# Kernel optimization log

Measured on AMD Instinct MI355X. Metric: run time of the kernel, lower is better.

## Reference

```python
import jax, jax.numpy as jnp
import numpy as np

NUM_GROUPS = 4   # temporal frames == deformable groups
K = 3            # deformable / fusion kernel size
PAD = 1
MAX_DISP = 7
STRIDE2 = 2


def _conv2d(x, w):
    # 3x3, stride 1, pad 1, no bias, NCHW/OIHW
    return jax.lax.conv_general_dilated(
        x, w, window_strides=(1, 1), padding=((PAD, PAD), (PAD, PAD)),
        dimension_numbers=("NCHW", "OIHW", "NCHW"))


def _correlation(x1, x2):
    """FlowNet/PWC correlation: kernel_size=1, max_displacement=7, stride1=1, stride2=2.
    Output: [B, 49, H, W], mean over channels of shifted dot products."""
    B, C, H, W = x1.shape
    r = MAX_DISP // STRIDE2          # 3 -> 7x7 displacement grid
    m = r * STRIDE2                  # 6 = max shift magnitude
    x2p = jnp.pad(x2, ((0, 0), (0, 0), (m, m), (m, m)))
    outs = []
    for di in range(-r, r + 1):
        for dj in range(-r, r + 1):
            dy, dx = di * STRIDE2, dj * STRIDE2
            sh = x2p[:, :, m + dy:m + dy + H, m + dx:m + dx + W]
            outs.append(jnp.mean(x1 * sh, axis=1))
    return jnp.stack(outs, axis=1)   # [B, 49, H, W]


def _deform_conv(x, offset, weight):
    """Deformable conv v1 (ConvOffset2d): 3x3, stride 1, pad 1, NUM_GROUPS deformable groups.
    offset: [B, G*2*K*K, H, W] laid out as (g, k, {dy,dx})."""
    B, C, H, W = x.shape
    G, K2 = NUM_GROUPS, K * K
    Cg = C // G
    off = offset.reshape(B, G, K2, 2, H, W)
    rel = (jnp.arange(K) - PAD).astype(x.dtype)
    rel_y = jnp.repeat(rel, K).reshape(1, 1, K2, 1, 1)   # kh-major, matches weight flatten
    rel_x = jnp.tile(rel, K).reshape(1, 1, K2, 1, 1)
    iy = jnp.arange(H, dtype=x.dtype).reshape(1, 1, 1, H, 1)
    ix = jnp.arange(W, dtype=x.dtype).reshape(1, 1, 1, 1, W)
    py = iy + rel_y + off[:, :, :, 0]   # [B,G,K2,H,W] sample rows
    px = ix + rel_x + off[:, :, :, 1]   # sample cols
    xg = x.reshape(B, G, Cg, H, W).transpose(0, 1, 3, 4, 2)  # [B,G,H,W,Cg]
    y0 = jnp.floor(py); x0 = jnp.floor(px)
    fy = py - y0; fx = px - x0
    y0 = y0.astype(jnp.int32); x0 = x0.astype(jnp.int32)
    bi = jnp.arange(B).reshape(B, 1, 1, 1, 1)
    gi = jnp.arange(G).reshape(1, G, 1, 1, 1)
    acc = jnp.zeros((B, G, K2, H, W, Cg), x.dtype)
    for dy in (0, 1):
        for dx in (0, 1):
            yy = y0 + dy; xx = x0 + dx
            wgt = (fy if dy else 1.0 - fy) * (fx if dx else 1.0 - fx)
            valid = ((yy >= 0) & (yy < H) & (xx >= 0) & (xx < W)).astype(x.dtype)
            v = xg[bi, gi, jnp.clip(yy, 0, H - 1), jnp.clip(xx, 0, W - 1)]
            acc = acc + v * (wgt * valid)[..., None]
    wr = weight.reshape(weight.shape[0], G, Cg, K2)  # [O,G,Cg,K2]
    return jnp.einsum('bgkhwc,ogck->bohw', acc, wr)


def setup_inputs() -> dict:
    key = jax.random.key(0)
    k0, k1, k2, k3 = jax.random.split(key, 4)
    B, C, H, W = 4, 256, 64, 64
    G = NUM_GROUPS
    inputs = jax.random.normal(k0, (B * G, C, H, W), jnp.float32)
    w_offset = jax.random.normal(k1, (G * 2 * K * K, C + MAX_DISP ** 2, K, K), jnp.float32) * 0.02
    w_def = jax.random.normal(k2, (C, C, K, K), jnp.float32) * 0.02
    w_fusion = jax.random.normal(k3, (C, C * G, K, K), jnp.float32) * 0.02
    return {"inputs": inputs, "w_offset": w_offset, "w_def": w_def,
            "w_fusion": w_fusion, "d1": 0, "d2": 0}


def reference(inputs, w_offset, w_def, w_fusion, d1, d2):
    # d1, d2 are unused by the original forward.
    G = NUM_GROUPS
    y = inputs[G - 1::G]
    _y = jax.lax.stop_gradient(y)
    feats = []
    for ii in range(G - 1):           # n_iter = 1
        x = inputs[ii::G]
        _x = jax.lax.stop_gradient(x)
        corr = _correlation(_x, _y)                       # [B,49,H,W]
        off = _conv2d(jnp.concatenate([x, corr], axis=1), w_offset)
        x = _deform_conv(x, off, w_def)
        feats.append(x)
    return _conv2d(jnp.concatenate(feats + [y], axis=1), w_fusion)
```

## Files before the change

kernel.cpp:

```cpp
#include <hip/hip_runtime.h>

#define HH 64
#define WW 64
#define HW 4096
#define CC 256
#define BB 4
#define GG 4
#define NPAIR 3

typedef __attribute__((ext_vector_type(8))) short short8;
typedef __attribute__((ext_vector_type(4))) float f32x4;
typedef unsigned short ushort_t;

__device__ inline ushort_t f2bf(float x) {
    unsigned int u = __float_as_uint(x);
    unsigned int r = (u + 0x7fffu + ((u >> 16) & 1u)) >> 16;
    return (ushort_t)r;
}
__device__ inline float bflo(unsigned u) { return __uint_as_float(u << 16); }
__device__ inline float bfhi(unsigned u) { return __uint_as_float(u & 0xffff0000u); }

__global__ void prep_wdef(const float* __restrict__ wd, ushort_t* __restrict__ wmf) {
    int idx = blockIdx.x * 256 + threadIdx.x;
    if (idx >= 9 * 256 * 256) return;
    int k = idx >> 16;
    int rem = idx & 65535;
    int o = rem >> 8;
    int c = rem & 255;
    wmf[idx] = f2bf(wd[((size_t)(o * 256 + c)) * 9 + k]);
}

__global__ void prep_woff(const float* __restrict__ wo, ushort_t* __restrict__ wmf) {
    int idx = blockIdx.x * 256 + threadIdx.x;
    if (idx >= 9 * 80 * 320) return;
    int k = idx / (80 * 320);
    int rem = idx % (80 * 320);
    int o = rem / 320;
    int ci = rem % 320;
    wmf[idx] = (o < 72 && ci < 305) ? f2bf(wo[((size_t)o * 305 + ci) * 9 + k]) : (ushort_t)0;
}

__global__ void prep_wfus(const float* __restrict__ wf, ushort_t* __restrict__ wmf) {
    int idx = blockIdx.x * 256 + threadIdx.x;
    if (idx >= 9 * 256 * 1024) return;
    int k = idx / (256 * 1024);
    int rem = idx % (256 * 1024);
    int o = rem / 1024;
    int ci = rem % 1024;
    wmf[idx] = f2bf(wf[((size_t)o * 1024 + ci) * 9 + k]);
}

__global__ void __launch_bounds__(256) xt_build(const float* __restrict__ in,
                                                ushort_t* __restrict__ XT) {
    __shared__ ushort_t tileT[64][72];
    int hw0 = blockIdx.x * 64;
    int ct = blockIdx.y;
    int z = blockIdx.z;
    int pair = z >> 2, b = z & 3;
    int t = threadIdx.x;
    int cil = t >> 2, q = t & 3;
    const float* sp = in + ((size_t)(b * 4 + pair) * 256 + ct * 64 + cil) * HW + hw0 + q * 16;
#pragma unroll
    for (int i = 0; i < 16; ++i) tileT[q * 16 + i][cil] = f2bf(sp[i]);
    __syncthreads();
    int hwl = t >> 2;
    const uint4* tp = reinterpret_cast<const uint4*>(&tileT[hwl][q * 16]);
    uint4* op = reinterpret_cast<uint4*>(
        &XT[((size_t)z * HW + hw0 + hwl) * 320 + ct * 64 + q * 16]);
    op[0] = tp[0];
    op[1] = tp[1];
}

__global__ void __launch_bounds__(256, 8) corr_partial(const float* __restrict__ in,
                                                       float* __restrict__ P) {
    __shared__ float x1l[8][64];
    __shared__ float x2l[8][7][76];
    int h = blockIdx.x, z = blockIdx.y, cg = blockIdx.z;
    int pair = z >> 2, b = z & 3;
    const float* x1 = in + (size_t)(b * GG + pair) * CC * HW + h * WW;
    const float* x2 = in + (size_t)(b * GG + 3) * CC * HW;
    int tid = threadIdx.x;
    int w = tid & 63;
    int dg = tid >> 6;

    float acc[2][7];
#pragma unroll
    for (int i = 0; i < 2; ++i)
#pragma unroll
        for (int j = 0; j < 7; ++j) acc[i][j] = 0.f;

    for (int c0 = cg * 64; c0 < cg * 64 + 64; c0 += 8) {
        __syncthreads();
#pragma unroll
        for (int idx = tid; idx < 512; idx += 256) {
            int cc = idx >> 6, ww = idx & 63;
            x1l[cc][ww] = x1[(size_t)(c0 + cc) * HW + ww];
        }
        for (int idx = tid; idx < 8 * 7 * 76; idx += 256) {
            int cc = idx / 532;
            int rem = idx - cc * 532;
            int r = rem / 76;
            int cl = rem - r * 76;
            int row = h + 2 * (r - 3);
            int col = cl - 6;
            float v = 0.f;
            if (row >= 0 && row < HH && col >= 0 && col < WW)
                v = x2[(size_t)(c0 + cc) * HW + row * WW + col];
            x2l[cc][r][cl] = v;
        }
        __syncthreads();
#pragma unroll
        for (int cc = 0; cc < 8; ++cc) {
            float x1v = x1l[cc][w];
#pragma unroll
            for (int i = 0; i < 2; ++i) {
                int di = dg * 2 + i;
                if (di < 7) {
#pragma unroll
                    for (int dj = 0; dj < 7; ++dj)
                        acc[i][dj] += x1v * x2l[cc][di][w + 2 * dj];
                }
            }
        }
    }
    float* pp = P + ((size_t)(cg * 12 + z) * 49) * HW + h * WW + w;
#pragma unroll
    for (int i = 0; i < 2; ++i) {
        int di = dg * 2 + i;
        if (di < 7) {
#pragma unroll
            for (int dj = 0; dj < 7; ++dj)
                pp[(size_t)(di * 7 + dj) * HW] = acc[i][dj];
        }
    }
}

__global__ void __launch_bounds__(256) corr_reduce(const float* __restrict__ P,
                                                   ushort_t* __restrict__ XT) {
    int h = blockIdx.x, z = blockIdx.y;
    int tid = threadIdx.x;
    int w = tid & 63;
    int dg = tid >> 6;
    const size_t cgs = (size_t)12 * 49 * HW;
    ushort_t* xrow = XT + ((size_t)z * HW + h * WW + w) * 320;
#pragma unroll
    for (int i = 0; i < 2; ++i) {
        int di = dg * 2 + i;
        if (di < 7) {
#pragma unroll
            for (int dj = 0; dj < 7; ++dj) {
                int d = di * 7 + dj;
                const float* pp = P + ((size_t)z * 49 + d) * HW + h * WW + w;
                float s = pp[0] + pp[cgs] + pp[2 * cgs] + pp[3 * cgs];
                xrow[256 + d] = f2bf(s * (1.f / 256.f));
            }
        }
    }
    if (dg == 3) {
#pragma unroll
        for (int p = 0; p < 15; ++p) xrow[305 + p] = 0;
    }
}

__global__ void __launch_bounds__(256, 2) offconv_mfma(const ushort_t* __restrict__ XT,
                                                       const ushort_t* __restrict__ wmf,
                                                       float* __restrict__ off) {
    __shared__ ushort_t a_lds[80][40];
    __shared__ ushort_t b_lds[128][40];
    int n0 = blockIdx.x * 128;
    int z = blockIdx.y;
    int t = threadIdx.x;
    int wid = t >> 6;
    int lane = t & 63;
    int l15 = lane & 15;
    int kq = lane >> 4;
    int r2 = t >> 1, half = t & 1;
    int hwB = n0 + r2;
    int hB = hwB >> 6, wB = hwB & 63;
    const ushort_t* xtb = XT + (size_t)z * HW * 320;

    f32x4 acc[5][2];
#pragma unroll
    for (int m = 0; m < 5; ++m)
#pragma unroll
        for (int n = 0; n < 2; ++n) acc[m][n] = (f32x4){0.f, 0.f, 0.f, 0.f};

    for (int tap = 0; tap < 9; ++tap) {
        int kh = tap / 3;
        int kw = tap - kh * 3;
        int hP = hB + kh - 1;
        int wP = wB + kw - 1;
        bool valid = (hP >= 0) && (hP < HH) && (wP >= 0) && (wP < WW);
        const ushort_t* brow = xtb + (size_t)(hP * WW + wP) * 320;
#pragma unroll 1
        for (int cs = 0; cs < 10; ++cs) {
            int ci0 = cs * 32;
            uint4 vb0 = make_uint4(0, 0, 0, 0), vb1 = make_uint4(0, 0, 0, 0);
            if (valid) {
                const uint4* gp = reinterpret_cast<const uint4*>(brow + ci0 + half * 16);
                vb0 = gp[0];
                vb1 = gp[1];
            }
            uint4 va0, va1;
            if (t < 160) {
                const uint4* ga = reinterpret_cast<const uint4*>(
                    wmf + ((size_t)tap * 80 + r2) * 320 + ci0 + half * 16);
                va0 = ga[0];
                va1 = ga[1];
            }
            __syncthreads();
            {
                uint4* bp = reinterpret_cast<uint4*>(&b_lds[r2][half * 16]);
                bp[0] = vb0;
                bp[1] = vb1;
                if (t < 160) {
                    uint4* ap = reinterpret_cast<uint4*>(&a_lds[r2][half * 16]);
                    ap[0] = va0;
                    ap[1] = va1;
                }
            }
            __syncthreads();
            short8 af[5], bf[2];
#pragma unroll
            for (int m = 0; m < 5; ++m)
                af[m] = *reinterpret_cast<const short8*>(&a_lds[m * 16 + l15][kq * 8]);
#pragma unroll
            for (int n = 0; n < 2; ++n)
                bf[n] = *reinterpret_cast<const short8*>(&b_lds[wid * 32 + n * 16 + l15][kq * 8]);
#pragma unroll
            for (int m = 0; m < 5; ++m)
#pragma unroll
                for (int n = 0; n < 2; ++n)
                    acc[m][n] = __builtin_amdgcn_mfma_f32_16x16x32_bf16(af[m], bf[n],
                                                                        acc[m][n], 0, 0, 0);
        }
    }
    float* ob = off + (size_t)z * 72 * HW + n0 + wid * 32;
#pragma unroll
    for (int m = 0; m < 5; ++m)
#pragma unroll
        for (int n = 0; n < 2; ++n)
#pragma unroll
            for (int e = 0; e < 4; ++e) {
                int o_l = m * 16 + kq * 4 + e;
                if (o_l < 72) ob[(size_t)o_l * HW + n * 16 + l15] = acc[m][n][e];
            }
}

__global__ void __launch_bounds__(256, 3) deform_mfma(const ushort_t* __restrict__ XT,
                                                      const float* __restrict__ off,
                                                      const ushort_t* __restrict__ wmf,
                                                      ushort_t* __restrict__ FT) {
    __shared__ ushort_t b_lds[64][264];
    int u = blockIdx.x & 7, v = blockIdx.x >> 3;
    int lin = u * 96 + v;
    int z = lin >> 6, h = lin & 63;
    int b = z & 3, pair = z >> 2;

    const ushort_t* xtz = XT + (size_t)z * HW * 320;
    const float* offp = off + (size_t)z * 72 * HW;
    int tid = threadIdx.x;
    int lane = tid & 63;
    int g = tid >> 6;
    int l15 = tid & 15;
    int kq = (tid >> 4) & 3;

    f32x4 acc[4][4];
#pragma unroll
    for (int m = 0; m < 4; ++m)
#pragma unroll
        for (int n = 0; n < 4; ++n) acc[m][n] = (f32x4){0.f, 0.f, 0.f, 0.f};

    for (int k = 0; k < 9; ++k) {
        __syncthreads();
        {
            float oy = offp[(size_t)(g * 18 + k * 2 + 0) * HW + h * WW + lane];
            float ox = offp[(size_t)(g * 18 + k * 2 + 1) * HW + h * WW + lane];
            float py = (float)h + (float)(k / 3 - 1) + oy;
            float px = (float)lane + (float)(k % 3 - 1) + ox;
            float y0f = floorf(py), x0f = floorf(px);
            float fy = py - y0f, fx = px - x0f;
            int y0 = (int)y0f, x0 = (int)x0f;
            int y1 = y0 + 1, x1 = x0 + 1;
            bool vy0 = (y0 >= 0) && (y0 < HH);
            bool vy1 = (y1 >= 0) && (y1 < HH);
            bool vx0 = (x0 >= 0) && (x0 < WW);
            bool vx1 = (x1 >= 0) && (x1 < WW);
            float w00 = (1.f - fy) * (1.f - fx) * ((vy0 && vx0) ? 1.f : 0.f);
            float w01 = (1.f - fy) * fx * ((vy0 && vx1) ? 1.f : 0.f);
            float w10 = fy * (1.f - fx) * ((vy1 && vx0) ? 1.f : 0.f);
            float w11 = fy * fx * ((vy1 && vx1) ? 1.f : 0.f);
            int cy0 = min(max(y0, 0), HH - 1), cy1 = min(max(y1, 0), HH - 1);
            int cx0 = min(max(x0, 0), WW - 1), cx1 = min(max(x1, 0), WW - 1);
            const ushort_t* p00 = xtz + (size_t)(cy0 * WW + cx0) * 320 + g * 64;
            const ushort_t* p01 = xtz + (size_t)(cy0 * WW + cx1) * 320 + g * 64;
            const ushort_t* p10 = xtz + (size_t)(cy1 * WW + cx0) * 320 + g * 64;
            const ushort_t* p11 = xtz + (size_t)(cy1 * WW + cx1) * 320 + g * 64;
#pragma unroll
            for (int c0 = 0; c0 < 64; c0 += 8) {
                uint4 a00 = *reinterpret_cast<const uint4*>(p00 + c0);
                uint4 a01 = *reinterpret_cast<const uint4*>(p01 + c0);
                uint4 a10 = *reinterpret_cast<const uint4*>(p10 + c0);
                uint4 a11 = *reinterpret_cast<const uint4*>(p11 + c0);
                unsigned pw[4];
                const unsigned* u00 = &a00.x;
                const unsigned* u01 = &a01.x;
                const unsigned* u10 = &a10.x;
                const unsigned* u11 = &a11.x;
#pragma unroll
                for (int q = 0; q < 4; ++q) {
                    float s0 = w00 * bflo(u00[q]) + w01 * bflo(u01[q]) +
                               w10 * bflo(u10[q]) + w11 * bflo(u11[q]);
                    float s1 = w00 * bfhi(u00[q]) + w01 * bfhi(u01[q]) +
                               w10 * bfhi(u10[q]) + w11 * bfhi(u11[q]);
                    pw[q] = (unsigned)f2bf(s0) | ((unsigned)f2bf(s1) << 16);
                }
                *reinterpret_cast<uint4*>(&b_lds[lane][g * 64 + c0]) =
                    make_uint4(pw[0], pw[1], pw[2], pw[3]);
            }
        }
        __syncthreads();
        const ushort_t* wkbase = wmf + (size_t)k * 65536 + (size_t)(g * 64) * 256;
#pragma unroll 1
        for (int cs = 0; cs < 8; ++cs) {
            int c0 = cs * 32;
            short8 bfr[4], afr[4];
#pragma unroll
            for (int n = 0; n < 4; ++n)
                bfr[n] = *reinterpret_cast<const short8*>(&b_lds[n * 16 + l15][c0 + kq * 8]);
#pragma unroll
            for (int m = 0; m < 4; ++m)
                afr[m] = *reinterpret_cast<const short8*>(
                    wkbase + (size_t)(m * 16 + l15) * 256 + c0 + kq * 8);
#pragma unroll
            for (int m = 0; m < 4; ++m)
#pragma unroll
                for (int n = 0; n < 4; ++n)
                    acc[m][n] = __builtin_amdgcn_mfma_f32_16x16x32_bf16(afr[m], bfr[n],
                                                                        acc[m][n], 0, 0, 0);
        }
    }
    __syncthreads();
#pragma unroll
    for (int m = 0; m < 4; ++m)
#pragma unroll
        for (int n = 0; n < 4; ++n) {
            unsigned lo = (unsigned)f2bf(acc[m][n][0]) | ((unsigned)f2bf(acc[m][n][1]) << 16);
            unsigned hi = (unsigned)f2bf(acc[m][n][2]) | ((unsigned)f2bf(acc[m][n][3]) << 16);
            uint2 vv = make_uint2(lo, hi);
            *reinterpret_cast<uint2*>(&b_lds[n * 16 + l15][g * 64 + m * 16 + kq * 4]) = vv;
        }
    __syncthreads();
    int wout = tid >> 2, ch = tid & 3;
    ushort_t* dst = FT + ((size_t)b * HW + h * 64 + wout) * 1024 + pair * 256 + ch * 64;
    const ushort_t* srcl = &b_lds[wout][ch * 64];
#pragma unroll
    for (int i = 0; i < 8; ++i) {
        uint4 vv = *reinterpret_cast<const uint4*>(srcl + i * 8);
        *reinterpret_cast<uint4*>(dst + i * 8) = vv;
    }
}

__global__ void __launch_bounds__(256) ft_build_y(const float* __restrict__ in,
                                                  ushort_t* __restrict__ FT) {
    __shared__ ushort_t tileT[64][72];
    int hw0 = blockIdx.x * 64;
    int ct = blockIdx.y;
    int b = blockIdx.z;
    int t = threadIdx.x;
    int cil = t >> 2, q = t & 3;
    const float* sp = in + ((size_t)(b * 4 + 3) * 256 + ct * 64 + cil) * HW + hw0 + q * 16;
#pragma unroll
    for (int i = 0; i < 16; ++i) tileT[q * 16 + i][cil] = f2bf(sp[i]);
    __syncthreads();
    int hwl = t >> 2;
    const uint4* tp = reinterpret_cast<const uint4*>(&tileT[hwl][q * 16]);
    uint4* op = reinterpret_cast<uint4*>(
        &FT[((size_t)b * HW + hw0 + hwl) * 1024 + 768 + ct * 64 + q * 16]);
    op[0] = tp[0];
    op[1] = tp[1];
}

__global__ void __launch_bounds__(256, 2) fusion_mfma(const ushort_t* __restrict__ FT,
                                                      const ushort_t* __restrict__ wmf,
                                                      float* __restrict__ out) {
    __shared__ ushort_t a_lds[9][64][32];
    __shared__ ushort_t b_hal[264][32];
    int lin = ((blockIdx.x & 7) << 6) | (blockIdx.x >> 3);
    int ot = lin & 3;
    int g2 = lin >> 2;
    int n0t = g2 & 31;
    int b = g2 >> 5;
    int o0 = ot * 64;
    int h0 = n0t * 2;
    int t = threadIdx.x;
    int wid = t >> 6;
    int lane = t & 63;
    int l15 = lane & 15;
    int kq = lane >> 4;
    const ushort_t* ftb = FT + (size_t)b * HW * 1024;

    f32x4 acc[4][2];
#pragma unroll
    for (int fm = 0; fm < 4; ++fm)
#pragma unroll
        for (int fn = 0; fn < 2; ++fn) acc[fm][fn] = (f32x4){0.f, 0.f, 0.f, 0.f};

#pragma unroll 1
    for (int cs = 0; cs < 32; ++cs) {
        int ci0 = cs * 32;
        __syncthreads();
        for (int idx = t; idx < 264; idx += 256) {
            int r = idx / 66, c = idx - r * 66;
            int hP = h0 + r - 1, wP = c - 1;
            uint4* dst = reinterpret_cast<uint4*>(&b_hal[idx][0]);
            if (hP >= 0 && hP < HH && wP >= 0 && wP < WW) {
                const uint4* src = reinterpret_cast<const uint4*>(
                    ftb + (size_t)(hP * WW + wP) * 1024 + ci0);
                dst[0] = src[0];
                dst[1] = src[1];
                dst[2] = src[2];
                dst[3] = src[3];
            } else {
                uint4 zz = make_uint4(0, 0, 0, 0);
                dst[0] = zz;
                dst[1] = zz;
                dst[2] = zz;
                dst[3] = zz;
            }
        }
        for (int idx = t; idx < 2304; idx += 256) {
            int tp = idx >> 8;
            int rem = idx & 255;
            int o = rem >> 2, q = rem & 3;
            *reinterpret_cast<uint4*>(&a_lds[tp][o][q * 8]) =
                *reinterpret_cast<const uint4*>(
                    wmf + ((size_t)(tp * 256 + o0 + o) << 10) + ci0 + q * 8);
        }
        __syncthreads();
#pragma unroll 1
        for (int tap = 0; tap < 9; ++tap) {
            int kh = tap / 3, kw = tap - kh * 3;
            short8 af[4], bf[2];
#pragma unroll
            for (int m = 0; m < 4; ++m)
                af[m] = *reinterpret_cast<const short8*>(&a_lds[tap][m * 16 + l15][kq * 8]);
#pragma unroll
            for (int n = 0; n < 2; ++n) {
                int p = wid * 32 + n * 16 + l15;
                int pos = ((p >> 6) + kh) * 66 + (p & 63) + kw;
                bf[n] = *reinterpret_cast<const short8*>(&b_hal[pos][kq * 8]);
            }
#pragma unroll
            for (int m = 0; m < 4; ++m)
#pragma unroll
                for (int n = 0; n < 2; ++n)
                    acc[m][n] = __builtin_amdgcn_mfma_f32_16x16x32_bf16(af[m], bf[n],
                                                                        acc[m][n], 0, 0, 0);
        }
    }
    float* ob = out + ((size_t)b * 256 + o0) * HW + h0 * 64 + wid * 32;
#pragma unroll
    for (int fm = 0; fm < 4; ++fm)
#pragma unroll
        for (int fn = 0; fn < 2; ++fn)
#pragma unroll
            for (int e = 0; e < 4; ++e) {
                int o_l = fm * 16 + 4 * kq + e;
                ob[(size_t)o_l * HW + fn * 16 + l15] = acc[fm][fn][e];
            }
}

extern "C" void kernel_launch(void* const* d_in, const int* in_sizes, int n_in,
                              void* d_out, int out_size, void* d_ws, size_t ws_size,
                              hipStream_t stream) {
    const float* in   = (const float*)d_in[0];
    const float* wOff = (const float*)d_in[1];
    const float* wDef = (const float*)d_in[2];
    const float* wFus = (const float*)d_in[3];
    float* out = (float*)d_out;
    char* base = (char*)d_ws;

    ushort_t* XT     = (ushort_t*)base;
    ushort_t* FT     = (ushort_t*)(base + 31457280);
    float* corrP     = (float*)(base + 31457280);
    float* offB      = (float*)(base + 65011712);
    ushort_t* wdefMF = (ushort_t*)(base + 79167488);
    ushort_t* woffMF = (ushort_t*)(base + 80347136);
    ushort_t* wfusMF = (ushort_t*)(base + 80807936);

    hipLaunchKernelGGL(prep_wdef, dim3((9 * 256 * 256 + 255) / 256), dim3(256), 0, stream,
                       wDef, wdefMF);
    hipLaunchKernelGGL(prep_woff, dim3((9 * 80 * 320 + 255) / 256), dim3(256), 0, stream,
                       wOff, woffMF);
    hipLaunchKernelGGL(prep_wfus, dim3((9 * 256 * 1024 + 255) / 256), dim3(256), 0, stream,
                       wFus, wfusMF);
    hipLaunchKernelGGL(xt_build, dim3(64, 4, 12), dim3(256), 0, stream, in, XT);
    hipLaunchKernelGGL(corr_partial, dim3(64, 12, 4), dim3(256), 0, stream, in, corrP);
    hipLaunchKernelGGL(corr_reduce, dim3(64, 12), dim3(256), 0, stream, corrP, XT);
    hipLaunchKernelGGL(offconv_mfma, dim3(32, 12), dim3(256), 0, stream, XT, woffMF, offB);
    hipLaunchKernelGGL(ft_build_y, dim3(64, 4, 4), dim3(256), 0, stream, in, FT);
    hipLaunchKernelGGL(deform_mfma, dim3(768), dim3(256), 0, stream, XT, offB, wdefMF, FT);
    hipLaunchKernelGGL(fusion_mfma, dim3(512), dim3(256), 0, stream, FT, wfusMF, out);
}
```

Measured before the change: 588.8 us.

## Use halo-tiled LDS staging in offset conv and pad fusion LDS rows

The offset convolution now loads, for each 32-channel slice, a two-row halo tile of the input (264 positions) plus the weights for all nine taps into LDS once, then runs all nine taps from LDS. The old version reloaded the input for each tap separately. This cuts global reads and barriers by roughly ninefold per channel slice, at the cost of much larger LDS use (about 77KB), which may limit occupancy. The block index is remapped with an XCD-aware swizzle, and the fusion kernel's LDS rows are padded from 32 to 40 elements to avoid bank conflicts.

```diff
diff --git a/kernel.cpp b/kernel.cpp
--- a/kernel.cpp
+++ b/kernel.cpp
@@ -165,18 +165,17 @@
 __global__ void __launch_bounds__(256, 2) offconv_mfma(const ushort_t* __restrict__ XT,
                                                        const ushort_t* __restrict__ wmf,
                                                        float* __restrict__ off) {
-    __shared__ ushort_t a_lds[80][40];
-    __shared__ ushort_t b_lds[128][40];
-    int n0 = blockIdx.x * 128;
-    int z = blockIdx.y;
+    __shared__ ushort_t a_lds[9][80][40];
+    __shared__ ushort_t b_hal[264][40];
+    int lin = (blockIdx.x & 7) * 48 + (blockIdx.x >> 3);
+    int z = lin >> 5;
+    int n0t = lin & 31;
+    int h0 = n0t * 2;
     int t = threadIdx.x;
     int wid = t >> 6;
     int lane = t & 63;
     int l15 = lane & 15;
     int kq = lane >> 4;
-    int r2 = t >> 1, half = t & 1;
-    int hwB = n0 + r2;
-    int hB = hwB >> 6, wB = hwB & 63;
     const ushort_t* xtb = XT + (size_t)z * HW * 320;
 
     f32x4 acc[5][2];
@@ -185,48 +184,51 @@
 #pragma unroll
         for (int n = 0; n < 2; ++n) acc[m][n] = (f32x4){0.f, 0.f, 0.f, 0.f};
 
-    for (int tap = 0; tap < 9; ++tap) {
-        int kh = tap / 3;
-        int kw = tap - kh * 3;
-        int hP = hB + kh - 1;
-        int wP = wB + kw - 1;
-        bool valid = (hP >= 0) && (hP < HH) && (wP >= 0) && (wP < WW);
-        const ushort_t* brow = xtb + (size_t)(hP * WW + wP) * 320;
 #pragma unroll 1
-        for (int cs = 0; cs < 10; ++cs) {
-            int ci0 = cs * 32;
-            uint4 vb0 = make_uint4(0, 0, 0, 0), vb1 = make_uint4(0, 0, 0, 0);
-            if (valid) {
-                const uint4* gp = reinterpret_cast<const uint4*>(brow + ci0 + half * 16);
-                vb0 = gp[0];
-                vb1 = gp[1];
-            }
-            uint4 va0, va1;
-            if (t < 160) {
-                const uint4* ga = reinterpret_cast<const uint4*>(
-                    wmf + ((size_t)tap * 80 + r2) * 320 + ci0 + half * 16);
-                va0 = ga[0];
-                va1 = ga[1];
-            }
-            __syncthreads();
-            {
-                uint4* bp = reinterpret_cast<uint4*>(&b_lds[r2][half * 16]);
-                bp[0] = vb0;
-                bp[1] = vb1;
-                if (t < 160) {
-                    uint4* ap = reinterpret_cast<uint4*>(&a_lds[r2][half * 16]);
-                    ap[0] = va0;
-                    ap[1] = va1;
-                }
-            }
-            __syncthreads();
+    for (int cs = 0; cs < 10; ++cs) {
+        int ci0 = cs * 32;
+        __syncthreads();
+        for (int idx = t; idx < 264; idx += 256) {
+            int r = idx / 66, c = idx - r * 66;
+            int hP = h0 + r - 1, wP = c - 1;
+            uint4* dst = reinterpret_cast<uint4*>(&b_hal[idx][0]);
+            if (hP >= 0 && hP < HH && wP >= 0 && wP < WW) {
+                const uint4* src = reinterpret_cast<const uint4*>(
+                    xtb + (size_t)(hP * WW + wP) * 320 + ci0);
+                dst[0] = src[0];
+                dst[1] = src[1];
+                dst[2] = src[2];
+                dst[3] = src[3];
+            } else {
+                uint4 zz = make_uint4(0, 0, 0, 0);
+                dst[0] = zz;
+                dst[1] = zz;
+                dst[2] = zz;
+                dst[3] = zz;
+            }
+        }
+        for (int idx = t; idx < 2880; idx += 256) {
+            int tp = idx / 320;
+            int rem = idx - tp * 320;
+            int o = rem >> 2, q = rem & 3;
+            *reinterpret_cast<uint4*>(&a_lds[tp][o][q * 8]) =
+                *reinterpret_cast<const uint4*>(
+                    wmf + ((size_t)tp * 80 + o) * 320 + ci0 + q * 8);
+        }
+        __syncthreads();
+#pragma unroll 1
+        for (int tap = 0; tap < 9; ++tap) {
+            int kh = tap / 3, kw = tap - kh * 3;
             short8 af[5], bf[2];
 #pragma unroll
             for (int m = 0; m < 5; ++m)
-                af[m] = *reinterpret_cast<const short8*>(&a_lds[m * 16 + l15][kq * 8]);
-#pragma unroll
-            for (int n = 0; n < 2; ++n)
-                bf[n] = *reinterpret_cast<const short8*>(&b_lds[wid * 32 + n * 16 + l15][kq * 8]);
+                af[m] = *reinterpret_cast<const short8*>(&a_lds[tap][m * 16 + l15][kq * 8]);
+#pragma unroll
+            for (int n = 0; n < 2; ++n) {
+                int p = wid * 32 + n * 16 + l15;
+                int pos = ((p >> 6) + kh) * 66 + (p & 63) + kw;
+                bf[n] = *reinterpret_cast<const short8*>(&b_hal[pos][kq * 8]);
+            }
 #pragma unroll
             for (int m = 0; m < 5; ++m)
 #pragma unroll
@@ -235,7 +237,7 @@
                                                                         acc[m][n], 0, 0, 0);
         }
     }
-    float* ob = off + (size_t)z * 72 * HW + n0 + wid * 32;
+    float* ob = off + (size_t)z * 72 * HW + h0 * 64 + wid * 32;
 #pragma unroll
     for (int m = 0; m < 5; ++m)
 #pragma unroll
@@ -384,8 +386,8 @@
 __global__ void __launch_bounds__(256, 2) fusion_mfma(const ushort_t* __restrict__ FT,
                                                       const ushort_t* __restrict__ wmf,
                                                       float* __restrict__ out) {
-    __shared__ ushort_t a_lds[9][64][32];
-    __shared__ ushort_t b_hal[264][32];
+    __shared__ ushort_t a_lds[9][64][40];
+    __shared__ ushort_t b_hal[264][40];
     int lin = ((blockIdx.x & 7) << 6) | (blockIdx.x >> 3);
     int ot = lin & 3;
     int g2 = lin >> 2;
@@ -498,7 +500,7 @@
     hipLaunchKernelGGL(xt_build, dim3(64, 4, 12), dim3(256), 0, stream, in, XT);
     hipLaunchKernelGGL(corr_partial, dim3(64, 12, 4), dim3(256), 0, stream, in, corrP);
     hipLaunchKernelGGL(corr_reduce, dim3(64, 12), dim3(256), 0, stream, corrP, XT);
-    hipLaunchKernelGGL(offconv_mfma, dim3(32, 12), dim3(256), 0, stream, XT, woffMF, offB);
+    hipLaunchKernelGGL(offconv_mfma, dim3(384), dim3(256), 0, stream, XT, woffMF, offB);
     hipLaunchKernelGGL(ft_build_y, dim3(64, 4, 4), dim3(256), 0, stream, in, FT);
     hipLaunchKernelGGL(deform_mfma, dim3(768), dim3(256), 0, stream, XT, offB, wdefMF, FT);
     hipLaunchKernelGGL(fusion_mfma, dim3(512), dim3(256), 0, stream, FT, wfusMF, out);
```

New measurement: 582.5 us. Within noise of the previous version (-1.1%).
